# Performance work log

Hardware: AMD Instinct MI355X
Metric: run time of the kernel (lower is better)

The kernel has to match this reference:

```python
import jax, jax.numpy as jnp
from jax import lax
import numpy as np

T, B, D, H = 2048, 64, 512, 512  # time, batch, input_size, hidden_size


def setup_inputs() -> dict:
    key = jax.random.key(0)
    k1, k2, k3, k4, k5 = jax.random.split(key, 5)
    s = 1.0 / np.sqrt(H)
    inputs = jax.random.normal(k1, (T, B, D), dtype=jnp.float32)
    W_ih = jax.random.uniform(k2, (4 * H, D), minval=-s, maxval=s, dtype=jnp.float32)
    W_hh = jax.random.uniform(k3, (4 * H, H), minval=-s, maxval=s, dtype=jnp.float32)
    b_ih = jax.random.uniform(k4, (4 * H,), minval=-s, maxval=s, dtype=jnp.float32)
    b_hh = jax.random.uniform(k5, (4 * H,), minval=-s, maxval=s, dtype=jnp.float32)
    return {"inputs": inputs, "W_ih": W_ih, "W_hh": W_hh, "b_ih": b_ih, "b_hh": b_hh}


def reference(inputs, W_ih, W_hh, b_ih, b_hh):
    # TimeRecurrentCell with batch_first=False, lstm=True, no attention, no reverse:
    # hidden=None -> zero-initialized (h, c); loop over time feeding an LSTM cell,
    # stacking per-step outputs along the time dim. Expressed as lax.scan.
    hidden = W_hh.shape[1]
    batch = inputs.shape[1]
    h0 = jnp.zeros((batch, hidden), dtype=inputs.dtype)
    c0 = jnp.zeros((batch, hidden), dtype=inputs.dtype)

    def step(carry, x_t):  # x_t: [B, D]
        h, c = carry
        gates = x_t @ W_ih.T + b_ih + h @ W_hh.T + b_hh  # [B, 4H]
        i, f, g, o = jnp.split(gates, 4, axis=-1)  # torch LSTMCell gate order
        i = jax.nn.sigmoid(i)
        f = jax.nn.sigmoid(f)
        g = jnp.tanh(g)
        o = jax.nn.sigmoid(o)
        c_new = f * c + i * g
        h_new = o * jnp.tanh(c_new)
        return (h_new, c_new), h_new

    (h_T, c_T), outputs = lax.scan(step, (h0, c0), inputs)  # outputs: [T, B, H]
    return outputs, (h_T, c_T)
```

## Files before the change

kernel.cpp:

```cpp
#include <hip/hip_runtime.h>
#include <hip/hip_bf16.h>
#include <hip/hip_fp16.h>

#define TT 2048
#define BB 64
#define HH 512
#define GG 2048

typedef __attribute__((ext_vector_type(4))) float f32x4;
typedef __attribute__((ext_vector_type(8))) short short8;
typedef __attribute__((ext_vector_type(4))) short short4v;
typedef __attribute__((ext_vector_type(4))) unsigned u32x4;

static __device__ __forceinline__ short f2bf(float f) {
  unsigned u = __builtin_bit_cast(unsigned, f);
  u = (u + 0x7FFFu + ((u >> 16) & 1u)) >> 16;
  return (short)u;
}
static __device__ __forceinline__ float fsigmoid(float x) { return 1.0f / (1.0f + __expf(-x)); }
static __device__ __forceinline__ float ftanh(float x) {
  float e = __expf(2.0f * x);
  return 1.0f - 2.0f / (e + 1.0f);
}
static __device__ __forceinline__ float h2f(unsigned short u) {
  __half h = __builtin_bit_cast(__half, u);
  return __half2float(h);
}

__global__ void cvt_bf16_kernel(const float4* __restrict__ in, short4v* __restrict__ outp, long n4) {
  long i = (long)blockIdx.x * blockDim.x + threadIdx.x;
  long stride = (long)gridDim.x * blockDim.x;
  for (; i < n4; i += stride) {
    float4 v = in[i];
    short4v o;
    o[0] = f2bf(v.x); o[1] = f2bf(v.y); o[2] = f2bf(v.z); o[3] = f2bf(v.w);
    outp[i] = o;
  }
}

__global__ void init_flags(unsigned* flags) {
  __hip_atomic_store(flags + threadIdx.x, 0u, __ATOMIC_RELAXED, __HIP_MEMORY_SCOPE_AGENT);
}

__global__ __launch_bounds__(256) void gemm_xpart(
    const __hip_bfloat16* __restrict__ Abf, const __hip_bfloat16* __restrict__ Bbf,
    const float* __restrict__ bih, const float* __restrict__ bhh, __half* __restrict__ xout) {
  __shared__ __hip_bfloat16 As[128 * 64];
  __shared__ __hip_bfloat16 Bs[128 * 64];
  const int nwg = gridDim.x;
  const int bid = blockIdx.x;
  const int vb = (bid & 7) * (nwg >> 3) + (bid >> 3);
  const int mt = vb >> 4;
  const int nt = vb & 15;
  const size_t m0 = (size_t)mt * 128;
  const int n0 = nt * 128;
  const int tid = threadIdx.x;
  const int lane = tid & 63;
  const int w = tid >> 6;
  const int wm = w >> 1, wn = w & 1;
  const int g = lane >> 4;
  f32x4 acc[4][4] = {};
  for (int k0 = 0; k0 < 512; k0 += 64) {
#pragma unroll
    for (int i = 0; i < 4; i++) {
      const int slot = w * 4 + i;
      const int row = slot * 8 + (lane >> 3);
      const int segS = (lane & 7) ^ (row & 7);
      const __hip_bfloat16* ga = Abf + (m0 + row) * 512 + k0 + segS * 8;
      const __hip_bfloat16* gb = Bbf + (size_t)(n0 + row) * 512 + k0 + segS * 8;
      __builtin_amdgcn_global_load_lds(
          (const __attribute__((address_space(1))) unsigned*)(const void*)ga,
          (__attribute__((address_space(3))) unsigned*)(void*)(As + slot * 512), 16, 0, 0);
      __builtin_amdgcn_global_load_lds(
          (const __attribute__((address_space(1))) unsigned*)(const void*)gb,
          (__attribute__((address_space(3))) unsigned*)(void*)(Bs + slot * 512), 16, 0, 0);
    }
    __syncthreads();
#pragma unroll
    for (int kk = 0; kk < 2; kk++) {
      short8 av[4], bv[4];
#pragma unroll
      for (int f = 0; f < 4; f++) {
        const int row = wm * 64 + f * 16 + (lane & 15);
        av[f] = *(const short8*)(As + row * 64 + ((((kk << 2) + g) ^ (row & 7)) << 3));
      }
#pragma unroll
      for (int f = 0; f < 4; f++) {
        const int row = wn * 64 + f * 16 + (lane & 15);
        bv[f] = *(const short8*)(Bs + row * 64 + ((((kk << 2) + g) ^ (row & 7)) << 3));
      }
#pragma unroll
      for (int fi = 0; fi < 4; fi++)
#pragma unroll
        for (int fj = 0; fj < 4; fj++)
          acc[fi][fj] = __builtin_amdgcn_mfma_f32_16x16x32_bf16(av[fi], bv[fj], acc[fi][fj], 0, 0, 0);
    }
    __syncthreads();
  }
#pragma unroll
  for (int fj = 0; fj < 4; fj++) {
    const int n = n0 + wn * 64 + fj * 16 + (lane & 15);
    const float bias = bih[n] + bhh[n];
    const int q = n >> 9;
    const int hcol = n & 511;
    const int cpn = hcol >> 5;
    const int j = hcol & 31;
    const int wv = (j >> 2) & 3;
    const int g4v = j & 3;
    const int slot = j >> 4;
    const int thr = wv * 64 + g4v * 16;
#pragma unroll
    for (int fi = 0; fi < 4; fi++) {
      const size_t mrow = m0 + wm * 64 + fi * 16 + g * 4;
#pragma unroll
      for (int r = 0; r < 4; r++) {
        const size_t m = mrow + r;
        const size_t tt = m >> 6;
        const int bglob = (int)(m & 63);
        const int bgn = bglob >> 4;
        const int b16n = bglob & 15;
        const size_t idx = ((((tt * 4 + bgn) * 16 + cpn) * 256 + (size_t)(thr + b16n)) << 3) +
                           (size_t)(slot * 4 + q);
        xout[idx] = __float2half(acc[fi][fj][r] + bias);
      }
    }
  }
}

__global__ __launch_bounds__(256, 1) void lstm_scan_kernel(
    const __half* __restrict__ xpart, const float* __restrict__ Whh,
    char* hbuf, float* __restrict__ outp, unsigned* flags) {
  __shared__ char Hs[16384];
  const int blk = blockIdx.x;
  const int bg = blk >> 4;
  const int cp = blk & 15;
  const int tid = threadIdx.x;
  const int lane = tid & 63;
  const int w = tid >> 6;
  const int b16 = lane & 15;
  const int g4 = lane >> 4;
  const int qr = b16 & 3;
  const int jj = b16 >> 2;
  const int colA = cp * 32 + w * 4 + g4;
  const int colB = cp * 32 + (w + 4) * 4 + g4;
  const int batchg = bg * 16 + b16;

  const int rowA = qr * 512 + cp * 32 + w * 4 + jj;
  const int rowB = qr * 512 + cp * 32 + (w + 4) * 4 + jj;
  short8 wA[16], wB[16];
#pragma unroll
  for (int kt = 0; kt < 16; kt++) {
    const float* pa = Whh + (size_t)rowA * 512 + kt * 32 + g4 * 8;
    const float* pb = Whh + (size_t)rowB * 512 + kt * 32 + g4 * 8;
    float4 a0 = *(const float4*)pa;
    float4 a1 = *(const float4*)(pa + 4);
    float4 b0 = *(const float4*)pb;
    float4 b1 = *(const float4*)(pb + 4);
    short8 va, vb;
    va[0] = f2bf(a0.x); va[1] = f2bf(a0.y); va[2] = f2bf(a0.z); va[3] = f2bf(a0.w);
    va[4] = f2bf(a1.x); va[5] = f2bf(a1.y); va[6] = f2bf(a1.z); va[7] = f2bf(a1.w);
    vb[0] = f2bf(b0.x); vb[1] = f2bf(b0.y); vb[2] = f2bf(b0.z); vb[3] = f2bf(b0.w);
    vb[4] = f2bf(b1.x); vb[5] = f2bf(b1.y); vb[6] = f2bf(b1.z); vb[7] = f2bf(b1.w);
    wA[kt] = va;
    wB[kt] = vb;
  }

  const size_t xstride = (size_t)4 * 16 * 256 * 8;
  const __half* xbase = xpart + ((size_t)bg * 16 + cp) * 256 * 8 + (size_t)tid * 8;
  short8 xv = *(const short8*)(const void*)xbase;

  const unsigned long long hroot = (unsigned long long)(uintptr_t)hbuf + (unsigned long long)(bg * 16384);

  float cA = 0.f, cB = 0.f, hAv = 0.f, hBv = 0.f;

  for (int t = 0; t < TT; t++) {
    const int tn = (t + 1 < TT) ? (t + 1) : (TT - 1);
    short8 xvn = *(const short8*)(const void*)(xbase + (size_t)tn * xstride);

    f32x4 accA = {0.f, 0.f, 0.f, 0.f};
    f32x4 accB = {0.f, 0.f, 0.f, 0.f};
    if (t > 0) {
      if (w == 0) {
        unsigned f;
        do {
          f = __hip_atomic_load(flags + bg * 16 + (lane & 15), __ATOMIC_RELAXED, __HIP_MEMORY_SCOPE_AGENT);
        } while (!__all((int)(f >= (unsigned)t)));
      }
      __syncthreads();
      const unsigned long long hb = hroot + (unsigned long long)((t & 1) * 65536);
      u32x4 hv[4];
#pragma unroll
      for (int p = 0; p < 4; p++) {
        const unsigned long long a = hb + (unsigned long long)((p * 4 + w) * 1024 + lane * 16);
        asm volatile("global_load_dwordx4 %0, %1, off sc0 sc1" : "=v"(hv[p]) : "v"(a));
      }
      asm volatile("s_waitcnt vmcnt(0)" ::: "memory");
      __builtin_amdgcn_sched_barrier(0);
#pragma unroll
      for (int p = 0; p < 4; p++) {
        const int b = p * 4 + w;
        *(u32x4*)(Hs + b * 1024 + ((lane ^ (b & 7)) << 4)) = hv[p];
      }
      __syncthreads();
#pragma unroll
      for (int kt = 0; kt < 16; kt++) {
        const int sp = ((kt * 4 + g4) ^ (b16 & 7));
        short8 hf = *(const short8*)(Hs + b16 * 1024 + (sp << 4));
        accA = __builtin_amdgcn_mfma_f32_16x16x32_bf16(wA[kt], hf, accA, 0, 0, 0);
        accB = __builtin_amdgcn_mfma_f32_16x16x32_bf16(wB[kt], hf, accB, 0, 0, 0);
      }
    }

    float iA = fsigmoid(accA[0] + h2f((unsigned short)xv[0]));
    float fA = fsigmoid(accA[1] + h2f((unsigned short)xv[1]));
    float gA = ftanh(accA[2] + h2f((unsigned short)xv[2]));
    float oA = fsigmoid(accA[3] + h2f((unsigned short)xv[3]));
    cA = fA * cA + iA * gA;
    hAv = oA * ftanh(cA);
    float iB = fsigmoid(accB[0] + h2f((unsigned short)xv[4]));
    float fB = fsigmoid(accB[1] + h2f((unsigned short)xv[5]));
    float gB = ftanh(accB[2] + h2f((unsigned short)xv[6]));
    float oB = fsigmoid(accB[3] + h2f((unsigned short)xv[7]));
    cB = fB * cB + iB * gB;
    hBv = oB * ftanh(cB);

    float hAp = __shfl_xor(hAv, 16, 64);
    float hBp = __shfl_xor(hBv, 16, 64);
    if ((g4 & 1) == 0) {
      unsigned* hd = (unsigned*)(hbuf + ((t + 1) & 1) * 65536 + bg * 16384 + b16 * 1024);
      unsigned pkA = (unsigned)(unsigned short)f2bf(hAv) | ((unsigned)(unsigned short)f2bf(hAp) << 16);
      unsigned pkB = (unsigned)(unsigned short)f2bf(hBv) | ((unsigned)(unsigned short)f2bf(hBp) << 16);
      __hip_atomic_store(hd + (colA >> 1), pkA, __ATOMIC_RELAXED, __HIP_MEMORY_SCOPE_AGENT);
      __hip_atomic_store(hd + (colB >> 1), pkB, __ATOMIC_RELAXED, __HIP_MEMORY_SCOPE_AGENT);
    }
    asm volatile("s_waitcnt vmcnt(0)" ::: "memory");
    __syncthreads();
    if (tid == 0)
      __hip_atomic_store(flags + bg * 16 + cp, (unsigned)(t + 1), __ATOMIC_RELAXED, __HIP_MEMORY_SCOPE_AGENT);

    float* od = outp + ((size_t)t * BB + batchg) * HH;
    od[colA] = hAv;
    od[colB] = hBv;
    xv = xvn;
  }

  float* hT = outp + (size_t)TT * BB * HH;
  float* cT = hT + (size_t)BB * HH;
  hT[(size_t)batchg * HH + colA] = hAv;
  hT[(size_t)batchg * HH + colB] = hBv;
  cT[(size_t)batchg * HH + colA] = cA;
  cT[(size_t)batchg * HH + colB] = cB;
}

extern "C" void kernel_launch(void* const* d_in, const int* in_sizes, int n_in,
                              void* d_out, int out_size, void* d_ws, size_t ws_size,
                              hipStream_t stream) {
  (void)in_sizes; (void)n_in; (void)out_size; (void)ws_size;
  const float* x = (const float*)d_in[0];
  const float* Wih = (const float*)d_in[1];
  const float* Whh = (const float*)d_in[2];
  const float* bih = (const float*)d_in[3];
  const float* bhh = (const float*)d_in[4];
  float* outp = (float*)d_out;
  char* ws = (char*)d_ws;

  const size_t M = (size_t)TT * BB;
  size_t off = 0;
  auto take = [&](size_t sz) { size_t r = off; off = (off + sz + 255) & ~255ULL; return r; };
  const size_t xbf_o = take(M * 512 * 2);
  const size_t wih_o = take((size_t)GG * 512 * 2);
  const size_t hbuf_o = take(2 * 65536);
  const size_t flg_o = take(256);
  const size_t xpart_o = take(M * (size_t)GG * 2);

  __hip_bfloat16* xbf = (__hip_bfloat16*)(ws + xbf_o);
  __hip_bfloat16* wihbf = (__hip_bfloat16*)(ws + wih_o);
  __half* xpart = (__half*)(ws + xpart_o);

  hipMemsetAsync(ws + hbuf_o, 0, 2 * 65536, stream);
  init_flags<<<1, 64, 0, stream>>>((unsigned*)(ws + flg_o));
  cvt_bf16_kernel<<<4096, 256, 0, stream>>>((const float4*)x, (short4v*)xbf, (long)(M * 512 / 4));
  cvt_bf16_kernel<<<256, 256, 0, stream>>>((const float4*)Wih, (short4v*)wihbf, (long)((size_t)GG * 512 / 4));

  gemm_xpart<<<16384, 256, 0, stream>>>(xbf, wihbf, bih, bhh, xpart);
  lstm_scan_kernel<<<64, 256, 0, stream>>>(xpart, Whh, ws + hbuf_o, outp, (unsigned*)(ws + flg_o));
}
```

Baseline: 8.228 ms.

## Replace flag-based step barrier with tagged hidden-state words polled directly

Removes the per-step flag array, the wait-for-flags spin and the store-drain-plus-barrier before publishing the flag. Each bf16 hidden value is now stored in a 32-bit word whose upper half holds the step number. Consumers poll the hidden buffer itself until every tag matches, then strip the tags with perm ops before writing to LDS. This cuts a round trip and a block barrier from the critical path of each recurrent step, but doubles the hidden-state traffic and adds retry loads while polling.

```diff
diff --git a/kernel.cpp b/kernel.cpp
--- a/kernel.cpp
+++ b/kernel.cpp
@@ -36,10 +36,6 @@
     o[0] = f2bf(v.x); o[1] = f2bf(v.y); o[2] = f2bf(v.z); o[3] = f2bf(v.w);
     outp[i] = o;
   }
-}
-
-__global__ void init_flags(unsigned* flags) {
-  __hip_atomic_store(flags + threadIdx.x, 0u, __ATOMIC_RELAXED, __HIP_MEMORY_SCOPE_AGENT);
 }
 
 __global__ __launch_bounds__(256) void gemm_xpart(
@@ -129,7 +125,7 @@
 
 __global__ __launch_bounds__(256, 1) void lstm_scan_kernel(
     const __half* __restrict__ xpart, const float* __restrict__ Whh,
-    char* hbuf, float* __restrict__ outp, unsigned* flags) {
+    char* hbufT, float* __restrict__ outp) {
   __shared__ char Hs[16384];
   const int blk = blockIdx.x;
   const int bg = blk >> 4;
@@ -169,7 +165,12 @@
   const __half* xbase = xpart + ((size_t)bg * 16 + cp) * 256 * 8 + (size_t)tid * 8;
   short8 xv = *(const short8*)(const void*)xbase;
 
-  const unsigned long long hroot = (unsigned long long)(uintptr_t)hbuf + (unsigned long long)(bg * 16384);
+  const unsigned long long hloadb =
+      (unsigned long long)(uintptr_t)hbufT + (unsigned long long)(bg * 32768) +
+      (unsigned long long)((tid >> 4) * 2048 + (tid & 15) * 128);
+  char* wdst = Hs + (tid >> 4) * 1024;
+  const int s0 = (tid & 15) * 4;
+  const int bb7 = (tid >> 4) & 7;
 
   float cA = 0.f, cB = 0.f, hAv = 0.f, hBv = 0.f;
 
@@ -180,26 +181,48 @@
     f32x4 accA = {0.f, 0.f, 0.f, 0.f};
     f32x4 accB = {0.f, 0.f, 0.f, 0.f};
     if (t > 0) {
-      if (w == 0) {
-        unsigned f;
-        do {
-          f = __hip_atomic_load(flags + bg * 16 + (lane & 15), __ATOMIC_RELAXED, __HIP_MEMORY_SCOPE_AGENT);
-        } while (!__all((int)(f >= (unsigned)t)));
-      }
-      __syncthreads();
-      const unsigned long long hb = hroot + (unsigned long long)((t & 1) * 65536);
-      u32x4 hv[4];
+      const unsigned long long hb = hloadb + (unsigned long long)((t & 1) * 131072);
+      const unsigned want = ((unsigned)t) << 16;
+      u32x4 hv[8];
+#pragma unroll
+      for (int k = 0; k < 8; k++)
+        asm volatile("global_load_dwordx4 %0, %1, off sc0 sc1"
+                     : "=v"(hv[k]) : "v"(hb + (unsigned long long)(k * 16)));
+      asm volatile("s_waitcnt vmcnt(0)" ::: "memory");
+      unsigned badk = 0;
+#pragma unroll
+      for (int k = 0; k < 8; k++) {
+        unsigned bad = ((hv[k][0] ^ want) | (hv[k][1] ^ want) | (hv[k][2] ^ want) |
+                        (hv[k][3] ^ want)) & 0xFFFF0000u;
+        badk |= (bad ? 1u : 0u) << k;
+      }
+      while (__any((int)badk)) {
+#pragma unroll
+        for (int k = 0; k < 8; k++)
+          if (badk & (1u << k))
+            asm volatile("global_load_dwordx4 %0, %1, off sc0 sc1"
+                         : "=v"(hv[k]) : "v"(hb + (unsigned long long)(k * 16)));
+        asm volatile("s_waitcnt vmcnt(0)" ::: "memory");
+        badk = 0;
+#pragma unroll
+        for (int k = 0; k < 8; k++) {
+          unsigned bad = ((hv[k][0] ^ want) | (hv[k][1] ^ want) | (hv[k][2] ^ want) |
+                          (hv[k][3] ^ want)) & 0xFFFF0000u;
+          badk |= (bad ? 1u : 0u) << k;
+        }
+      }
+      __builtin_amdgcn_sched_barrier(0);
+      unsigned ut[16];
+#pragma unroll
+      for (int i = 0; i < 16; i++) {
+        unsigned lo = hv[i >> 1][(i & 1) * 2];
+        unsigned hi = hv[i >> 1][(i & 1) * 2 + 1];
+        ut[i] = __builtin_amdgcn_perm(hi, lo, 0x05040100u);
+      }
 #pragma unroll
       for (int p = 0; p < 4; p++) {
-        const unsigned long long a = hb + (unsigned long long)((p * 4 + w) * 1024 + lane * 16);
-        asm volatile("global_load_dwordx4 %0, %1, off sc0 sc1" : "=v"(hv[p]) : "v"(a));
-      }
-      asm volatile("s_waitcnt vmcnt(0)" ::: "memory");
-      __builtin_amdgcn_sched_barrier(0);
-#pragma unroll
-      for (int p = 0; p < 4; p++) {
-        const int b = p * 4 + w;
-        *(u32x4*)(Hs + b * 1024 + ((lane ^ (b & 7)) << 4)) = hv[p];
+        u32x4 v = {ut[4 * p], ut[4 * p + 1], ut[4 * p + 2], ut[4 * p + 3]};
+        *(u32x4*)(wdst + (((s0 + p) ^ bb7) << 4)) = v;
       }
       __syncthreads();
 #pragma unroll
@@ -224,19 +247,20 @@
     cB = fB * cB + iB * gB;
     hBv = oB * ftanh(cB);
 
+    const unsigned tagS = ((unsigned)(t + 1)) << 16;
     float hAp = __shfl_xor(hAv, 16, 64);
     float hBp = __shfl_xor(hBv, 16, 64);
     if ((g4 & 1) == 0) {
-      unsigned* hd = (unsigned*)(hbuf + ((t + 1) & 1) * 65536 + bg * 16384 + b16 * 1024);
-      unsigned pkA = (unsigned)(unsigned short)f2bf(hAv) | ((unsigned)(unsigned short)f2bf(hAp) << 16);
-      unsigned pkB = (unsigned)(unsigned short)f2bf(hBv) | ((unsigned)(unsigned short)f2bf(hBp) << 16);
-      __hip_atomic_store(hd + (colA >> 1), pkA, __ATOMIC_RELAXED, __HIP_MEMORY_SCOPE_AGENT);
-      __hip_atomic_store(hd + (colB >> 1), pkB, __ATOMIC_RELAXED, __HIP_MEMORY_SCOPE_AGENT);
-    }
-    asm volatile("s_waitcnt vmcnt(0)" ::: "memory");
-    __syncthreads();
-    if (tid == 0)
-      __hip_atomic_store(flags + bg * 16 + cp, (unsigned)(t + 1), __ATOMIC_RELAXED, __HIP_MEMORY_SCOPE_AGENT);
+      char* hd = hbufT + ((t + 1) & 1) * 131072 + bg * 32768 + b16 * 2048;
+      unsigned dA0 = tagS | (unsigned)(unsigned short)f2bf(hAv);
+      unsigned dA1 = tagS | (unsigned)(unsigned short)f2bf(hAp);
+      unsigned dB0 = tagS | (unsigned)(unsigned short)f2bf(hBv);
+      unsigned dB1 = tagS | (unsigned)(unsigned short)f2bf(hBp);
+      unsigned long long uA = (unsigned long long)dA0 | ((unsigned long long)dA1 << 32);
+      unsigned long long uB = (unsigned long long)dB0 | ((unsigned long long)dB1 << 32);
+      __hip_atomic_store((unsigned long long*)(hd + colA * 4), uA, __ATOMIC_RELAXED, __HIP_MEMORY_SCOPE_AGENT);
+      __hip_atomic_store((unsigned long long*)(hd + colB * 4), uB, __ATOMIC_RELAXED, __HIP_MEMORY_SCOPE_AGENT);
+    }
 
     float* od = outp + ((size_t)t * BB + batchg) * HH;
     od[colA] = hAv;
@@ -269,19 +293,18 @@
   auto take = [&](size_t sz) { size_t r = off; off = (off + sz + 255) & ~255ULL; return r; };
   const size_t xbf_o = take(M * 512 * 2);
   const size_t wih_o = take((size_t)GG * 512 * 2);
-  const size_t hbuf_o = take(2 * 65536);
-  const size_t flg_o = take(256);
+  const size_t hbuf_o = take(2 * 131072);
   const size_t xpart_o = take(M * (size_t)GG * 2);
 
   __hip_bfloat16* xbf = (__hip_bfloat16*)(ws + xbf_o);
   __hip_bfloat16* wihbf = (__hip_bfloat16*)(ws + wih_o);
   __half* xpart = (__half*)(ws + xpart_o);
 
-  hipMemsetAsync(ws + hbuf_o, 0, 2 * 65536, stream);
-  init_flags<<<1, 64, 0, stream>>>((unsigned*)(ws + flg_o));
+  hipMemsetAsync(ws + hbuf_o, 0, 2 * 131072, stream);
+
   cvt_bf16_kernel<<<4096, 256, 0, stream>>>((const float4*)x, (short4v*)xbf, (long)(M * 512 / 4));
   cvt_bf16_kernel<<<256, 256, 0, stream>>>((const float4*)Wih, (short4v*)wihbf, (long)((size_t)GG * 512 / 4));
 
   gemm_xpart<<<16384, 256, 0, stream>>>(xbf, wihbf, bih, bhh, xpart);
-  lstm_scan_kernel<<<64, 256, 0, stream>>>(xpart, Whh, ws + hbuf_o, outp, (unsigned*)(ws + flg_o));
-}
+  lstm_scan_kernel<<<64, 256, 0, stream>>>(xpart, Whh, ws + hbuf_o, outp);
+}
```

Measured after the change: 11.08 ms. +34.7%, slower.

## Use per-wave flags to drop block barriers and split MFMA accumulator chains

Applied to the files above, without the earlier changes.

Replaces the per-block step flag with one flag per wave, so every wave polls all 64 flags of its batch group and publishes its own flag. This removes two __syncthreads from the recurrent step's critical path. The MFMA reduction is split into two independent accumulator chains to shorten the dependency chain, and the prefetch of the next x slice moves after the flag store. In exchange the flag array and its init grow, and each wave now spins on global memory.

```diff
diff --git a/kernel.cpp b/kernel.cpp
--- a/kernel.cpp
+++ b/kernel.cpp
@@ -169,24 +169,21 @@
   const __half* xbase = xpart + ((size_t)bg * 16 + cp) * 256 * 8 + (size_t)tid * 8;
   short8 xv = *(const short8*)(const void*)xbase;
 
-  const unsigned long long hroot = (unsigned long long)(uintptr_t)hbuf + (unsigned long long)(bg * 16384);
+  const unsigned long long hroot =
+      (unsigned long long)(uintptr_t)hbuf + (unsigned long long)(bg * 16384);
+  unsigned* fbase = flags + bg * 64;
+  const int myflag = cp * 4 + w;
 
   float cA = 0.f, cB = 0.f, hAv = 0.f, hBv = 0.f;
 
   for (int t = 0; t < TT; t++) {
-    const int tn = (t + 1 < TT) ? (t + 1) : (TT - 1);
-    short8 xvn = *(const short8*)(const void*)(xbase + (size_t)tn * xstride);
-
-    f32x4 accA = {0.f, 0.f, 0.f, 0.f};
-    f32x4 accB = {0.f, 0.f, 0.f, 0.f};
+    f32x4 accA0 = {0.f, 0.f, 0.f, 0.f}, accA1 = {0.f, 0.f, 0.f, 0.f};
+    f32x4 accB0 = {0.f, 0.f, 0.f, 0.f}, accB1 = {0.f, 0.f, 0.f, 0.f};
     if (t > 0) {
-      if (w == 0) {
-        unsigned f;
-        do {
-          f = __hip_atomic_load(flags + bg * 16 + (lane & 15), __ATOMIC_RELAXED, __HIP_MEMORY_SCOPE_AGENT);
-        } while (!__all((int)(f >= (unsigned)t)));
-      }
-      __syncthreads();
+      unsigned f;
+      do {
+        f = __hip_atomic_load(fbase + lane, __ATOMIC_RELAXED, __HIP_MEMORY_SCOPE_AGENT);
+      } while (!__all((int)(f >= (unsigned)t)));
       const unsigned long long hb = hroot + (unsigned long long)((t & 1) * 65536);
       u32x4 hv[4];
 #pragma unroll
@@ -203,13 +200,19 @@
       }
       __syncthreads();
 #pragma unroll
-      for (int kt = 0; kt < 16; kt++) {
-        const int sp = ((kt * 4 + g4) ^ (b16 & 7));
-        short8 hf = *(const short8*)(Hs + b16 * 1024 + (sp << 4));
-        accA = __builtin_amdgcn_mfma_f32_16x16x32_bf16(wA[kt], hf, accA, 0, 0, 0);
-        accB = __builtin_amdgcn_mfma_f32_16x16x32_bf16(wB[kt], hf, accB, 0, 0, 0);
-      }
-    }
+      for (int kt = 0; kt < 16; kt += 2) {
+        const int sp0 = ((kt * 4 + g4) ^ (b16 & 7));
+        const int sp1 = (((kt + 1) * 4 + g4) ^ (b16 & 7));
+        short8 hf0 = *(const short8*)(Hs + b16 * 1024 + (sp0 << 4));
+        short8 hf1 = *(const short8*)(Hs + b16 * 1024 + (sp1 << 4));
+        accA0 = __builtin_amdgcn_mfma_f32_16x16x32_bf16(wA[kt], hf0, accA0, 0, 0, 0);
+        accB0 = __builtin_amdgcn_mfma_f32_16x16x32_bf16(wB[kt], hf0, accB0, 0, 0, 0);
+        accA1 = __builtin_amdgcn_mfma_f32_16x16x32_bf16(wA[kt + 1], hf1, accA1, 0, 0, 0);
+        accB1 = __builtin_amdgcn_mfma_f32_16x16x32_bf16(wB[kt + 1], hf1, accB1, 0, 0, 0);
+      }
+    }
+    f32x4 accA = accA0 + accA1;
+    f32x4 accB = accB0 + accB1;
 
     float iA = fsigmoid(accA[0] + h2f((unsigned short)xv[0]));
     float fA = fsigmoid(accA[1] + h2f((unsigned short)xv[1]));
@@ -234,9 +237,11 @@
       __hip_atomic_store(hd + (colB >> 1), pkB, __ATOMIC_RELAXED, __HIP_MEMORY_SCOPE_AGENT);
     }
     asm volatile("s_waitcnt vmcnt(0)" ::: "memory");
-    __syncthreads();
-    if (tid == 0)
-      __hip_atomic_store(flags + bg * 16 + cp, (unsigned)(t + 1), __ATOMIC_RELAXED, __HIP_MEMORY_SCOPE_AGENT);
+    if (lane == 0)
+      __hip_atomic_store(fbase + myflag, (unsigned)(t + 1), __ATOMIC_RELAXED, __HIP_MEMORY_SCOPE_AGENT);
+
+    const int tn = (t + 1 < TT) ? (t + 1) : (TT - 1);
+    short8 xvn = *(const short8*)(const void*)(xbase + (size_t)tn * xstride);
 
     float* od = outp + ((size_t)t * BB + batchg) * HH;
     od[colA] = hAv;
@@ -270,7 +275,7 @@
   const size_t xbf_o = take(M * 512 * 2);
   const size_t wih_o = take((size_t)GG * 512 * 2);
   const size_t hbuf_o = take(2 * 65536);
-  const size_t flg_o = take(256);
+  const size_t flg_o = take(1024);
   const size_t xpart_o = take(M * (size_t)GG * 2);
 
   __hip_bfloat16* xbf = (__hip_bfloat16*)(ws + xbf_o);
@@ -278,7 +283,7 @@
   __half* xpart = (__half*)(ws + xpart_o);
 
   hipMemsetAsync(ws + hbuf_o, 0, 2 * 65536, stream);
-  init_flags<<<1, 64, 0, stream>>>((unsigned*)(ws + flg_o));
+  init_flags<<<1, 256, 0, stream>>>((unsigned*)(ws + flg_o));
   cvt_bf16_kernel<<<4096, 256, 0, stream>>>((const float4*)x, (short4v*)xbf, (long)(M * 512 / 4));
   cvt_bf16_kernel<<<256, 256, 0, stream>>>((const float4*)Wih, (short4v*)wihbf, (long)((size_t)GG * 512 / 4));
 
```

Result: slower. 11.58 ms (+40.7%).

## Halve scan workgroups to 32x512 threads and re-layout xpart for dword gate loads

Applied to the files above, without the earlier changes.

The recurrent scan now uses 32 workgroups of 512 threads, each owning 64 hidden columns, instead of 64 workgroups of 256. Each batch group therefore synchronizes 8 flags per step instead of 16, and each workgroup reads half as many h-chunks per step. The GEMM epilogue writes the precomputed input projections in a new layout so each thread fetches four dword loads per step, prefetched after the flag store. The changes aim to cut cross-workgroup synchronization and global traffic on the serial critical path. In exchange, each step does more per-workgroup LDS and MFMA work, and register pressure rises at 512 threads with 32 short8 weight registers per thread.

```diff
diff --git a/kernel.cpp b/kernel.cpp
--- a/kernel.cpp
+++ b/kernel.cpp
@@ -11,6 +11,7 @@
 typedef __attribute__((ext_vector_type(8))) short short8;
 typedef __attribute__((ext_vector_type(4))) short short4v;
 typedef __attribute__((ext_vector_type(4))) unsigned u32x4;
+typedef unsigned long long ull;
 
 static __device__ __forceinline__ short f2bf(float f) {
   unsigned u = __builtin_bit_cast(unsigned, f);
@@ -59,6 +60,7 @@
   const int w = tid >> 6;
   const int wm = w >> 1, wn = w & 1;
   const int g = lane >> 4;
+  const int l15 = lane & 15;
   f32x4 acc[4][4] = {};
   for (int k0 = 0; k0 < 512; k0 += 64) {
 #pragma unroll
@@ -81,12 +83,12 @@
       short8 av[4], bv[4];
 #pragma unroll
       for (int f = 0; f < 4; f++) {
-        const int row = wm * 64 + f * 16 + (lane & 15);
+        const int row = wm * 64 + f * 16 + l15;
         av[f] = *(const short8*)(As + row * 64 + ((((kk << 2) + g) ^ (row & 7)) << 3));
       }
 #pragma unroll
       for (int f = 0; f < 4; f++) {
-        const int row = wn * 64 + f * 16 + (lane & 15);
+        const int row = wn * 64 + f * 16 + l15;
         bv[f] = *(const short8*)(Bs + row * 64 + ((((kk << 2) + g) ^ (row & 7)) << 3));
       }
 #pragma unroll
@@ -97,43 +99,36 @@
     }
     __syncthreads();
   }
+  const int q = nt >> 2;
+  const int gt = mt * 2 + wm;
 #pragma unroll
   for (int fj = 0; fj < 4; fj++) {
-    const int n = n0 + wn * 64 + fj * 16 + (lane & 15);
+    const int n = n0 + wn * 64 + fj * 16 + l15;
     const float bias = bih[n] + bhh[n];
-    const int q = n >> 9;
-    const int hcol = n & 511;
-    const int cpn = hcol >> 5;
-    const int j = hcol & 31;
-    const int wv = (j >> 2) & 3;
-    const int g4v = j & 3;
-    const int slot = j >> 4;
-    const int thr = wv * 64 + g4v * 16;
+    const int cp = (nt & 3) * 2 + wn;
+    const int slot = fj >> 1;
+    const int wpart = (fj & 1) * 4 + (l15 >> 2);
+    const int g4s = l15 & 3;
 #pragma unroll
     for (int fi = 0; fi < 4; fi++) {
-      const size_t mrow = m0 + wm * 64 + fi * 16 + g * 4;
 #pragma unroll
       for (int r = 0; r < 4; r++) {
-        const size_t m = mrow + r;
-        const size_t tt = m >> 6;
-        const int bglob = (int)(m & 63);
-        const int bgn = bglob >> 4;
-        const int b16n = bglob & 15;
-        const size_t idx = ((((tt * 4 + bgn) * 16 + cpn) * 256 + (size_t)(thr + b16n)) << 3) +
-                           (size_t)(slot * 4 + q);
-        xout[idx] = __float2half(acc[fi][fj][r] + bias);
-      }
-    }
-  }
-}
-
-__global__ __launch_bounds__(256, 1) void lstm_scan_kernel(
+        const int b16 = g * 4 + r;
+        const int thr = wpart * 64 + g4s * 16 + b16;
+        const size_t hidx = ((((size_t)gt * 4 + q) * 4 + fi) * 8 + cp) * 1024 + thr * 2 + slot;
+        xout[hidx] = __float2half(acc[fi][fj][r] + bias);
+      }
+    }
+  }
+}
+
+__global__ __launch_bounds__(512, 2) void lstm_scan_kernel(
     const __half* __restrict__ xpart, const float* __restrict__ Whh,
     char* hbuf, float* __restrict__ outp, unsigned* flags) {
   __shared__ char Hs[16384];
   const int blk = blockIdx.x;
-  const int bg = blk >> 4;
-  const int cp = blk & 15;
+  const int bg = blk >> 3;
+  const int cp = blk & 7;
   const int tid = threadIdx.x;
   const int lane = tid & 63;
   const int w = tid >> 6;
@@ -141,12 +136,12 @@
   const int g4 = lane >> 4;
   const int qr = b16 & 3;
   const int jj = b16 >> 2;
-  const int colA = cp * 32 + w * 4 + g4;
-  const int colB = cp * 32 + (w + 4) * 4 + g4;
+  const int colA = cp * 64 + w * 4 + g4;
+  const int colB = cp * 64 + (w + 8) * 4 + g4;
   const int batchg = bg * 16 + b16;
 
-  const int rowA = qr * 512 + cp * 32 + w * 4 + jj;
-  const int rowB = qr * 512 + cp * 32 + (w + 4) * 4 + jj;
+  const int rowA = qr * 512 + cp * 64 + w * 4 + jj;
+  const int rowB = qr * 512 + cp * 64 + (w + 8) * 4 + jj;
   short8 wA[16], wB[16];
 #pragma unroll
   for (int kt = 0; kt < 16; kt++) {
@@ -165,40 +160,44 @@
     wB[kt] = vb;
   }
 
-  const size_t xstride = (size_t)4 * 16 * 256 * 8;
-  const __half* xbase = xpart + ((size_t)bg * 16 + cp) * 256 * 8 + (size_t)tid * 8;
-  short8 xv = *(const short8*)(const void*)xbase;
-
-  const unsigned long long hroot = (unsigned long long)(uintptr_t)hbuf + (unsigned long long)(bg * 16384);
+  const ull xroot = (ull)(uintptr_t)xpart + ((ull)(bg * 8 + cp) * 512 + (ull)tid) * 4ull;
+  const ull qstep = 4ull * 8 * 512 * 4;
+  const ull xstep = 4ull * qstep;
+  const ull hroot = (ull)(uintptr_t)hbuf + (ull)(bg * 16384);
+  unsigned* fbase = flags + bg * 8;
+
+  unsigned xq0, xq1, xq2, xq3, xn0, xn1, xn2, xn3;
+  asm volatile("global_load_dword %0, %1, off" : "=v"(xq0) : "v"(xroot));
+  asm volatile("global_load_dword %0, %1, off" : "=v"(xq1) : "v"(xroot + qstep));
+  asm volatile("global_load_dword %0, %1, off" : "=v"(xq2) : "v"(xroot + 2 * qstep));
+  asm volatile("global_load_dword %0, %1, off" : "=v"(xq3) : "v"(xroot + 3 * qstep));
+  asm volatile("s_waitcnt vmcnt(0)" ::: "memory");
 
   float cA = 0.f, cB = 0.f, hAv = 0.f, hBv = 0.f;
 
   for (int t = 0; t < TT; t++) {
-    const int tn = (t + 1 < TT) ? (t + 1) : (TT - 1);
-    short8 xvn = *(const short8*)(const void*)(xbase + (size_t)tn * xstride);
-
     f32x4 accA = {0.f, 0.f, 0.f, 0.f};
     f32x4 accB = {0.f, 0.f, 0.f, 0.f};
     if (t > 0) {
       if (w == 0) {
         unsigned f;
         do {
-          f = __hip_atomic_load(flags + bg * 16 + (lane & 15), __ATOMIC_RELAXED, __HIP_MEMORY_SCOPE_AGENT);
+          f = __hip_atomic_load(fbase + (lane & 7), __ATOMIC_RELAXED, __HIP_MEMORY_SCOPE_AGENT);
         } while (!__all((int)(f >= (unsigned)t)));
       }
       __syncthreads();
-      const unsigned long long hb = hroot + (unsigned long long)((t & 1) * 65536);
-      u32x4 hv[4];
-#pragma unroll
-      for (int p = 0; p < 4; p++) {
-        const unsigned long long a = hb + (unsigned long long)((p * 4 + w) * 1024 + lane * 16);
+      const ull hb = hroot + (ull)((t & 1) * 65536);
+      u32x4 hv[2];
+#pragma unroll
+      for (int p = 0; p < 2; p++) {
+        const ull a = hb + (ull)((p * 8 + w) * 1024 + lane * 16);
         asm volatile("global_load_dwordx4 %0, %1, off sc0 sc1" : "=v"(hv[p]) : "v"(a));
       }
       asm volatile("s_waitcnt vmcnt(0)" ::: "memory");
       __builtin_amdgcn_sched_barrier(0);
 #pragma unroll
-      for (int p = 0; p < 4; p++) {
-        const int b = p * 4 + w;
+      for (int p = 0; p < 2; p++) {
+        const int b = p * 8 + w;
         *(u32x4*)(Hs + b * 1024 + ((lane ^ (b & 7)) << 4)) = hv[p];
       }
       __syncthreads();
@@ -211,16 +210,16 @@
       }
     }
 
-    float iA = fsigmoid(accA[0] + h2f((unsigned short)xv[0]));
-    float fA = fsigmoid(accA[1] + h2f((unsigned short)xv[1]));
-    float gA = ftanh(accA[2] + h2f((unsigned short)xv[2]));
-    float oA = fsigmoid(accA[3] + h2f((unsigned short)xv[3]));
+    float iA = fsigmoid(accA[0] + h2f((unsigned short)(xq0 & 0xFFFF)));
+    float fA = fsigmoid(accA[1] + h2f((unsigned short)(xq1 & 0xFFFF)));
+    float gA = ftanh(accA[2] + h2f((unsigned short)(xq2 & 0xFFFF)));
+    float oA = fsigmoid(accA[3] + h2f((unsigned short)(xq3 & 0xFFFF)));
     cA = fA * cA + iA * gA;
     hAv = oA * ftanh(cA);
-    float iB = fsigmoid(accB[0] + h2f((unsigned short)xv[4]));
-    float fB = fsigmoid(accB[1] + h2f((unsigned short)xv[5]));
-    float gB = ftanh(accB[2] + h2f((unsigned short)xv[6]));
-    float oB = fsigmoid(accB[3] + h2f((unsigned short)xv[7]));
+    float iB = fsigmoid(accB[0] + h2f((unsigned short)(xq0 >> 16)));
+    float fB = fsigmoid(accB[1] + h2f((unsigned short)(xq1 >> 16)));
+    float gB = ftanh(accB[2] + h2f((unsigned short)(xq2 >> 16)));
+    float oB = fsigmoid(accB[3] + h2f((unsigned short)(xq3 >> 16)));
     cB = fB * cB + iB * gB;
     hBv = oB * ftanh(cB);
 
@@ -236,12 +235,18 @@
     asm volatile("s_waitcnt vmcnt(0)" ::: "memory");
     __syncthreads();
     if (tid == 0)
-      __hip_atomic_store(flags + bg * 16 + cp, (unsigned)(t + 1), __ATOMIC_RELAXED, __HIP_MEMORY_SCOPE_AGENT);
+      __hip_atomic_store(fbase + cp, (unsigned)(t + 1), __ATOMIC_RELAXED, __HIP_MEMORY_SCOPE_AGENT);
+
+    const ull pfb = xroot + (ull)(t + 1 < TT ? t + 1 : TT - 1) * xstep;
+    asm volatile("global_load_dword %0, %1, off" : "=v"(xn0) : "v"(pfb));
+    asm volatile("global_load_dword %0, %1, off" : "=v"(xn1) : "v"(pfb + qstep));
+    asm volatile("global_load_dword %0, %1, off" : "=v"(xn2) : "v"(pfb + 2 * qstep));
+    asm volatile("global_load_dword %0, %1, off" : "=v"(xn3) : "v"(pfb + 3 * qstep));
 
     float* od = outp + ((size_t)t * BB + batchg) * HH;
     od[colA] = hAv;
     od[colB] = hBv;
-    xv = xvn;
+    xq0 = xn0; xq1 = xn1; xq2 = xn2; xq3 = xn3;
   }
 
   float* hT = outp + (size_t)TT * BB * HH;
@@ -283,5 +288,5 @@
   cvt_bf16_kernel<<<256, 256, 0, stream>>>((const float4*)Wih, (short4v*)wihbf, (long)((size_t)GG * 512 / 4));
 
   gemm_xpart<<<16384, 256, 0, stream>>>(xbf, wihbf, bih, bhh, xpart);
-  lstm_scan_kernel<<<64, 256, 0, stream>>>(xpart, Whh, ws + hbuf_o, outp, (unsigned*)(ws + flg_o));
-}
+  lstm_scan_kernel<<<32, 512, 0, stream>>>(xpart, Whh, ws + hbuf_o, outp, (unsigned*)(ws + flg_o));
+}
```

New measurement: 7.857 ms. -4.5%, faster.
